# Kernel tuning notes

Hardware: AMD Instinct MI355X
Metric: run time of the kernel (lower is better)

## Reference

```python
import jax, jax.numpy as jnp
import numpy as np

B, S, D = 4, 2048, 1024
H, HD = 16, 64
FF = 4096
EPS = 1e-5
NEG = -1000000.0


def setup_inputs() -> dict:
    key = jax.random.key(0)
    ks = jax.random.split(key, 12)
    sc = lambda n: 1.0 / np.sqrt(n)
    return {
        "x": jax.random.normal(ks[0], (B, S, D), jnp.float32),
        "valid_lens": jax.random.randint(ks[1], (B,), 1, S, jnp.int32),
        "Wq": jax.random.normal(ks[2], (D, H * HD), jnp.float32) * sc(D),
        "Wk": jax.random.normal(ks[3], (D, H * HD), jnp.float32) * sc(D),
        "Wv": jax.random.normal(ks[4], (D, H * HD), jnp.float32) * sc(D),
        "Wo": jax.random.normal(ks[5], (H * HD, D), jnp.float32) * sc(H * HD),
        "W1": jax.random.normal(ks[6], (D, FF), jnp.float32) * sc(D),
        "b1": jnp.zeros((FF,), jnp.float32),
        "W2": jax.random.normal(ks[7], (FF, D), jnp.float32) * sc(FF),
        "b2": jnp.zeros((D,), jnp.float32),
        "g1": jnp.ones((D,), jnp.float32),
        "beta1": jnp.zeros((D,), jnp.float32),
        "g2": jnp.ones((D,), jnp.float32),
        "beta2": jnp.zeros((D,), jnp.float32),
    }


def _layernorm(x, g, b):
    mu = jnp.mean(x, axis=-1, keepdims=True)
    var = jnp.var(x, axis=-1, keepdims=True)
    return (x - mu) * jax.lax.rsqrt(var + EPS) * g + b


def _encoder_block(x, valid_lens, Wq, Wk, Wv, Wo, W1, b1, W2, b2, g1, beta1, g2, beta2):
    # multi-head attention (vectorized over heads; masked softmax as in original)
    q = (x @ Wq).reshape(B, S, H, HD)
    k = (x @ Wk).reshape(B, S, H, HD)
    v = (x @ Wv).reshape(B, S, H, HD)
    scores = jnp.einsum("bqhd,bkhd->bhqk", q, k) / np.sqrt(HD)
    # mask: key positions >= valid_len[b] set to -1e6 (matches python-loop masking)
    col = jnp.arange(S)[None, None, None, :]           # [1,1,1,S]
    mask = col < valid_lens[:, None, None, None]       # [B,1,1,S]
    scores = jnp.where(mask, scores, NEG)
    w = jax.nn.softmax(scores, axis=-1)
    attn = jnp.einsum("bhqk,bkhd->bqhd", w, v).reshape(B, S, H * HD)
    attn_out = attn @ Wo
    res1 = _layernorm(attn_out + x, g1, beta1)
    ff = jax.nn.relu(res1 @ W1 + b1) @ W2 + b2
    return _layernorm(ff + res1, g2, beta2)


def reference(x, valid_lens, Wq, Wk, Wv, Wo, W1, b1, W2, b2, g1, beta1, g2, beta2):
    return _encoder_block(x, valid_lens, Wq, Wk, Wv, Wo, W1, b1, W2, b2, g1, beta1, g2, beta2)
```

## Files before the change

kernel.cpp:

```cpp
#include <hip/hip_runtime.h>
#include <hip/hip_bf16.h>
#include <stdint.h>

#define BB 4
#define SS 2048
#define DD 1024
#define HH 16
#define HD 64
#define FF 4096
#define MM (BB * SS)
#define BH (BB * HH)

typedef __bf16 bf16x8 __attribute__((ext_vector_type(8)));
typedef float f32x4 __attribute__((ext_vector_type(4)));

static __device__ __forceinline__ unsigned short f2bf(float f) {
  union { float f; unsigned u; } v; v.f = f;
  unsigned r = v.u + 0x7fffu + ((v.u >> 16) & 1u);
  return (unsigned short)(r >> 16);
}

#define GLD_LDS16(SRC, DST)                                          \
  __builtin_amdgcn_global_load_lds(                                  \
      (const __attribute__((address_space(1))) void*)(SRC),          \
      (__attribute__((address_space(3))) void*)(DST), 16, 0, 0)

__global__ __launch_bounds__(256) void cast_bf16_k(const float* __restrict__ in,
                                                   unsigned short* __restrict__ out) {
  size_t i = ((size_t)blockIdx.x * 256 + threadIdx.x) * 4;
  float4 v = *(const float4*)(in + i);
  ushort4 u;
  u.x = f2bf(v.x); u.y = f2bf(v.y); u.z = f2bf(v.z); u.w = f2bf(v.w);
  *(ushort4*)(out + i) = u;
}

__global__ __launch_bounds__(256) void transpose_cast_k(const float* __restrict__ in,
                                                        unsigned short* __restrict__ out,
                                                        int K, int N) {
  __shared__ float tile[32][33];
  int n0 = blockIdx.x * 32, k0 = blockIdx.y * 32;
  int tx = threadIdx.x, ty = threadIdx.y;
#pragma unroll
  for (int i = 0; i < 32; i += 8)
    tile[ty + i][tx] = in[(size_t)(k0 + ty + i) * N + n0 + tx];
  __syncthreads();
#pragma unroll
  for (int i = 0; i < 32; i += 8)
    out[(size_t)(n0 + ty + i) * K + k0 + tx] = f2bf(tile[tx][ty + i]);
}

template <int EPI>
__global__ __launch_bounds__(256, 2) void gemm_bt(const unsigned short* __restrict__ A,
                                                  const unsigned short* __restrict__ BT,
                                                  const float* __restrict__ bias,
                                                  void* __restrict__ Cout,
                                                  int N, int K) {
  __shared__ __align__(16) unsigned short Al[128 * 64];
  __shared__ __align__(16) unsigned short Bl[128 * 64];
  const int t = threadIdx.x;
  const int w = t >> 6, l = t & 63, lr = l & 15, lg = l >> 4;
  const int brow = blockIdx.y << 7, bcol = blockIdx.x << 7;
  const int wr = w >> 1, wc = w & 1;
  f32x4 acc[4][4] = {};

  for (int kt = 0; kt < K; kt += 64) {
    __syncthreads();
#pragma unroll
    for (int is = 0; is < 4; ++is) {
      int c = is * 256 + t;
      int row = c >> 3;
      int js = (c & 7) ^ (row & 7);
      GLD_LDS16(A + (size_t)(brow + row) * K + kt + js * 8,
                &Al[(size_t)(is * 256 + w * 64) * 8]);
      GLD_LDS16(BT + (size_t)(bcol + row) * K + kt + js * 8,
                &Bl[(size_t)(is * 256 + w * 64) * 8]);
    }
    __syncthreads();
#pragma unroll
    for (int kk = 0; kk < 2; ++kk) {
      bf16x8 af[4], bfr[4];
#pragma unroll
      for (int m = 0; m < 4; ++m) {
        int row = wr * 64 + m * 16 + lr;
        af[m] = *(const bf16x8*)&Al[row * 64 + (((kk * 4 + lg) ^ (row & 7)) << 3)];
      }
#pragma unroll
      for (int n = 0; n < 4; ++n) {
        int row = wc * 64 + n * 16 + lr;
        bfr[n] = *(const bf16x8*)&Bl[row * 64 + (((kk * 4 + lg) ^ (row & 7)) << 3)];
      }
#pragma unroll
      for (int m = 0; m < 4; ++m)
#pragma unroll
        for (int n = 0; n < 4; ++n)
          acc[m][n] = __builtin_amdgcn_mfma_f32_16x16x32_bf16(af[m], bfr[n], acc[m][n], 0, 0, 0);
    }
  }

#pragma unroll
  for (int m = 0; m < 4; ++m) {
#pragma unroll
    for (int n = 0; n < 4; ++n) {
      int col = bcol + wc * 64 + n * 16 + lr;
      float bv = 0.f;
      if (EPI == 3 || EPI == 4) bv = bias[col];
#pragma unroll
      for (int i = 0; i < 4; ++i) {
        int row = brow + wr * 64 + m * 16 + lg * 4 + i;
        float v = acc[m][n][i];
        if (EPI == 0) {
          ((float*)Cout)[(size_t)row * N + col] = v;
        } else if (EPI == 1) {
          int b = row >> 11, s = row & 2047, h = col >> 6, hd = col & 63;
          ((unsigned short*)Cout)[(((size_t)(b * HH + h)) * SS + s) * HD + hd] = f2bf(v);
        } else if (EPI == 2) {
          int b = row >> 11, s = row & 2047, h = col >> 6, hd = col & 63;
          ((unsigned short*)Cout)[(((size_t)(b * HH + h)) * HD + hd) * SS + s] = f2bf(v);
        } else if (EPI == 3) {
          v += bv; v = v > 0.f ? v : 0.f;
          ((unsigned short*)Cout)[(size_t)row * N + col] = f2bf(v);
        } else {
          v += bv;
          ((float*)Cout)[(size_t)row * N + col] = v;
        }
      }
    }
  }
}

__global__ __launch_bounds__(256, 2) void attn_kernel(const unsigned short* __restrict__ Q,
                                                      const unsigned short* __restrict__ Kg,
                                                      const unsigned short* __restrict__ VT,
                                                      const int* __restrict__ vlens,
                                                      unsigned short* __restrict__ O) {
  __shared__ __align__(16) unsigned short Kt[64 * 64];
  __shared__ __align__(16) unsigned short Vt[64 * 64];
  __shared__ __align__(16) unsigned short Pt[4][16 * 64];
  const int t = threadIdx.x;
  const int w = t >> 6, l = t & 63, lr = l & 15, lg = l >> 4;
  const int bh = blockIdx.y, b = bh >> 4, h = bh & 15;
  const int q0 = blockIdx.x << 6;
  const int vl = vlens[b];
  const size_t base = (size_t)bh * SS * HD;

  bf16x8 qf[2];
  {
    const int qrow = q0 + w * 16 + lr;
    qf[0] = *(const bf16x8*)(Q + base + (size_t)qrow * HD + lg * 8);
    qf[1] = *(const bf16x8*)(Q + base + (size_t)qrow * HD + 32 + lg * 8);
  }
  f32x4 o[4] = {};
  float m_i[4], l_i[4];
#pragma unroll
  for (int i = 0; i < 4; ++i) { m_i[i] = -3.0e38f; l_i[i] = 0.f; }

  const int nkv = (vl + 63) >> 6;
  for (int kbi = 0; kbi < nkv; ++kbi) {
    const int kb = kbi << 6;
    __syncthreads();
#pragma unroll
    for (int is = 0; is < 2; ++is) {
      int c = is * 256 + t;
      int row = c >> 3;
      int js = (c & 7) ^ (row & 7);
      GLD_LDS16(Kg + base + (size_t)(kb + row) * HD + js * 8,
                &Kt[(is * 256 + w * 64) * 8]);
      GLD_LDS16(VT + base + (size_t)row * SS + kb + js * 8,
                &Vt[(is * 256 + w * 64) * 8]);
    }
    __syncthreads();

    f32x4 s[4] = {};
#pragma unroll
    for (int kk = 0; kk < 2; ++kk)
#pragma unroll
      for (int n = 0; n < 4; ++n) {
        int row = n * 16 + lr;
        bf16x8 kf = *(const bf16x8*)&Kt[row * 64 + (((kk * 4 + lg) ^ (row & 7)) << 3)];
        s[n] = __builtin_amdgcn_mfma_f32_16x16x32_bf16(qf[kk], kf, s[n], 0, 0, 0);
      }

#pragma unroll
    for (int i = 0; i < 4; ++i) {
      float rm = -3.0e38f;
#pragma unroll
      for (int n = 0; n < 4; ++n) {
        float sv = s[n][i] * 0.125f;
        if (kb + n * 16 + lr >= vl) sv = -3.0e38f;
        s[n][i] = sv;
        rm = fmaxf(rm, sv);
      }
      rm = fmaxf(rm, __shfl_xor(rm, 1));
      rm = fmaxf(rm, __shfl_xor(rm, 2));
      rm = fmaxf(rm, __shfl_xor(rm, 4));
      rm = fmaxf(rm, __shfl_xor(rm, 8));
      float mnew = fmaxf(m_i[i], rm);
      float alpha = __expf(m_i[i] - mnew);
      float rs = 0.f;
#pragma unroll
      for (int n = 0; n < 4; ++n) {
        float p = __expf(s[n][i] - mnew);
        s[n][i] = p;
        rs += p;
      }
      rs += __shfl_xor(rs, 1);
      rs += __shfl_xor(rs, 2);
      rs += __shfl_xor(rs, 4);
      rs += __shfl_xor(rs, 8);
      l_i[i] = l_i[i] * alpha + rs;
      m_i[i] = mnew;
#pragma unroll
      for (int n = 0; n < 4; ++n) o[n][i] *= alpha;
    }

#pragma unroll
    for (int n = 0; n < 4; ++n) {
      int colc = n * 2 + (lr >> 3);
      int cl = lr & 7;
#pragma unroll
      for (int i = 0; i < 4; ++i) {
        int row = lg * 4 + i;
        Pt[w][row * 64 + ((colc ^ (row & 7)) << 3) + cl] = f2bf(s[n][i]);
      }
    }
#pragma unroll
    for (int kk = 0; kk < 2; ++kk) {
      bf16x8 pf = *(const bf16x8*)&Pt[w][lr * 64 + (((kk * 4 + lg) ^ (lr & 7)) << 3)];
#pragma unroll
      for (int n = 0; n < 4; ++n) {
        int row = n * 16 + lr;
        bf16x8 vf = *(const bf16x8*)&Vt[row * 64 + (((kk * 4 + lg) ^ (row & 7)) << 3)];
        o[n] = __builtin_amdgcn_mfma_f32_16x16x32_bf16(pf, vf, o[n], 0, 0, 0);
      }
    }
  }

  float inv[4];
#pragma unroll
  for (int i = 0; i < 4; ++i) inv[i] = 1.f / l_i[i];
#pragma unroll
  for (int n = 0; n < 4; ++n)
#pragma unroll
    for (int i = 0; i < 4; ++i) {
      int qrow = q0 + w * 16 + lg * 4 + i;
      O[((size_t)b * SS + qrow) * DD + h * HD + n * 16 + lr] = f2bf(o[n][i] * inv[i]);
    }
}

__global__ __launch_bounds__(256) void ln_kernel(const float* __restrict__ a,
                                                 const float* __restrict__ bsrc,
                                                 const float* __restrict__ g,
                                                 const float* __restrict__ be,
                                                 float* __restrict__ outf,
                                                 unsigned short* __restrict__ outb) {
  const int row = blockIdx.x;
  const int t = threadIdx.x;
  const float4 av = ((const float4*)(a + (size_t)row * DD))[t];
  const float4 bv = ((const float4*)(bsrc + (size_t)row * DD))[t];
  float4 s;
  s.x = av.x + bv.x; s.y = av.y + bv.y; s.z = av.z + bv.z; s.w = av.w + bv.w;
  float sum = s.x + s.y + s.z + s.w;
  float sq = s.x * s.x + s.y * s.y + s.z * s.z + s.w * s.w;
#pragma unroll
  for (int mm = 1; mm < 64; mm <<= 1) {
    sum += __shfl_xor(sum, mm);
    sq += __shfl_xor(sq, mm);
  }
  __shared__ float red[8];
  const int w = t >> 6, l = t & 63;
  if (l == 0) { red[w] = sum; red[4 + w] = sq; }
  __syncthreads();
  sum = red[0] + red[1] + red[2] + red[3];
  sq = red[4] + red[5] + red[6] + red[7];
  const float mu = sum * (1.f / (float)DD);
  const float var = sq * (1.f / (float)DD) - mu * mu;
  const float rs = rsqrtf(var + 1e-5f);
  const float4 gv = ((const float4*)g)[t];
  const float4 bev = ((const float4*)be)[t];
  float4 y;
  y.x = (s.x - mu) * rs * gv.x + bev.x;
  y.y = (s.y - mu) * rs * gv.y + bev.y;
  y.z = (s.z - mu) * rs * gv.z + bev.z;
  y.w = (s.w - mu) * rs * gv.w + bev.w;
  if (outf) ((float4*)(outf + (size_t)row * DD))[t] = y;
  if (outb) {
    ushort4 u;
    u.x = f2bf(y.x); u.y = f2bf(y.y); u.z = f2bf(y.z); u.w = f2bf(y.w);
    ((ushort4*)(outb + (size_t)row * DD))[t] = u;
  }
}

extern "C" void kernel_launch(void* const* d_in, const int* in_sizes, int n_in,
                              void* d_out, int out_size, void* d_ws, size_t ws_size,
                              hipStream_t stream) {
  (void)in_sizes; (void)n_in; (void)out_size; (void)ws_size;
  const float* x = (const float*)d_in[0];
  const int* vlen = (const int*)d_in[1];
  const float* Wq = (const float*)d_in[2];
  const float* Wk = (const float*)d_in[3];
  const float* Wv = (const float*)d_in[4];
  const float* Wo = (const float*)d_in[5];
  const float* W1 = (const float*)d_in[6];
  const float* b1 = (const float*)d_in[7];
  const float* W2 = (const float*)d_in[8];
  const float* b2 = (const float*)d_in[9];
  const float* g1 = (const float*)d_in[10];
  const float* be1 = (const float*)d_in[11];
  const float* g2 = (const float*)d_in[12];
  const float* be2 = (const float*)d_in[13];
  float* out = (float*)d_out;

  char* ws = (char*)d_ws;
  size_t off = 0;
  auto alloc = [&](size_t bytes) {
    char* p = ws + off;
    off += (bytes + 255) & ~(size_t)255;
    return p;
  };
  unsigned short* xb = (unsigned short*)alloc((size_t)MM * DD * 2);
  unsigned short* WqT = (unsigned short*)alloc((size_t)DD * DD * 2);
  unsigned short* WkT = (unsigned short*)alloc((size_t)DD * DD * 2);
  unsigned short* WvT = (unsigned short*)alloc((size_t)DD * DD * 2);
  unsigned short* WoT = (unsigned short*)alloc((size_t)DD * DD * 2);
  unsigned short* W1T = (unsigned short*)alloc((size_t)FF * DD * 2);
  unsigned short* W2T = (unsigned short*)alloc((size_t)DD * FF * 2);
  unsigned short* Qb = (unsigned short*)alloc((size_t)MM * DD * 2);
  unsigned short* Kbb = (unsigned short*)alloc((size_t)MM * DD * 2);
  unsigned short* VTb = (unsigned short*)alloc((size_t)MM * DD * 2);
  unsigned short* attnb = (unsigned short*)alloc((size_t)MM * DD * 2);
  float* proj = (float*)alloc((size_t)MM * DD * 4);
  float* res1f = (float*)alloc((size_t)MM * DD * 4);
  unsigned short* res1b = (unsigned short*)alloc((size_t)MM * DD * 2);
  unsigned short* ff1 = Qb;
  float* ff2 = proj;

  cast_bf16_k<<<MM * DD / 1024, 256, 0, stream>>>(x, xb);
  transpose_cast_k<<<dim3(32, 32), dim3(32, 8), 0, stream>>>(Wq, WqT, DD, DD);
  transpose_cast_k<<<dim3(32, 32), dim3(32, 8), 0, stream>>>(Wk, WkT, DD, DD);
  transpose_cast_k<<<dim3(32, 32), dim3(32, 8), 0, stream>>>(Wv, WvT, DD, DD);
  transpose_cast_k<<<dim3(32, 32), dim3(32, 8), 0, stream>>>(Wo, WoT, DD, DD);
  transpose_cast_k<<<dim3(128, 32), dim3(32, 8), 0, stream>>>(W1, W1T, DD, FF);
  transpose_cast_k<<<dim3(32, 128), dim3(32, 8), 0, stream>>>(W2, W2T, FF, DD);

  gemm_bt<1><<<dim3(8, 64), 256, 0, stream>>>(xb, WqT, nullptr, Qb, DD, DD);
  gemm_bt<1><<<dim3(8, 64), 256, 0, stream>>>(xb, WkT, nullptr, Kbb, DD, DD);
  gemm_bt<2><<<dim3(8, 64), 256, 0, stream>>>(xb, WvT, nullptr, VTb, DD, DD);

  attn_kernel<<<dim3(SS / 64, BH), 256, 0, stream>>>(Qb, Kbb, VTb, vlen, attnb);

  gemm_bt<0><<<dim3(8, 64), 256, 0, stream>>>(attnb, WoT, nullptr, proj, DD, DD);
  ln_kernel<<<MM, 256, 0, stream>>>(proj, x, g1, be1, res1f, res1b);
  gemm_bt<3><<<dim3(32, 64), 256, 0, stream>>>(res1b, W1T, b1, ff1, FF, DD);
  gemm_bt<4><<<dim3(8, 64), 256, 0, stream>>>(ff1, W2T, b2, ff2, DD, FF);
  ln_kernel<<<MM, 256, 0, stream>>>(ff2, res1f, g2, be2, out, nullptr);
}
```

Measured before the change: 456.7 us.

## Fuse QKV projections into one GEMM and widen attention KV tiles with lazy rescaling

Replaces three separate Q/K/V projection GEMMs with one N=3072 GEMM whose epilogue scatters into the Q, K and transposed-V buffers, and folds the 1/sqrt(d) scale into Q. The attention kernel now processes 128-key blocks per iteration and applies the mask as an additive bias. It skips the online-softmax rescale unless the running max grows by more than 8. This cuts kernel launches, loop iterations and exp/multiply work. The fused GEMM assumes the three weight buffers and the three output buffers sit contiguously in memory.

```diff
diff --git a/kernel.cpp b/kernel.cpp
--- a/kernel.cpp
+++ b/kernel.cpp
@@ -110,18 +110,24 @@
         float v = acc[m][n][i];
         if (EPI == 0) {
           ((float*)Cout)[(size_t)row * N + col] = v;
-        } else if (EPI == 1) {
-          int b = row >> 11, s = row & 2047, h = col >> 6, hd = col & 63;
-          ((unsigned short*)Cout)[(((size_t)(b * HH + h)) * SS + s) * HD + hd] = f2bf(v);
-        } else if (EPI == 2) {
-          int b = row >> 11, s = row & 2047, h = col >> 6, hd = col & 63;
-          ((unsigned short*)Cout)[(((size_t)(b * HH + h)) * HD + hd) * SS + s] = f2bf(v);
         } else if (EPI == 3) {
           v += bv; v = v > 0.f ? v : 0.f;
           ((unsigned short*)Cout)[(size_t)row * N + col] = f2bf(v);
-        } else {
+        } else if (EPI == 4) {
           v += bv;
           ((float*)Cout)[(size_t)row * N + col] = v;
+        } else if (EPI == 5) {
+          int b = row >> 11, s = row & 2047;
+          int which = col >> 10, cin = col & 1023;
+          int h = cin >> 6, hd = cin & 63;
+          unsigned short* qb = (unsigned short*)Cout;
+          if (which == 0) {
+            qb[(((size_t)(b * HH + h)) * SS + s) * HD + hd] = f2bf(v * 0.125f);
+          } else if (which == 1) {
+            (qb + (size_t)MM * DD)[(((size_t)(b * HH + h)) * SS + s) * HD + hd] = f2bf(v);
+          } else {
+            (qb + 2 * (size_t)MM * DD)[(((size_t)(b * HH + h)) * HD + hd) * SS + s] = f2bf(v);
+          }
         }
       }
     }
@@ -133,9 +139,9 @@
                                                       const unsigned short* __restrict__ VT,
                                                       const int* __restrict__ vlens,
                                                       unsigned short* __restrict__ O) {
-  __shared__ __align__(16) unsigned short Kt[64 * 64];
-  __shared__ __align__(16) unsigned short Vt[64 * 64];
-  __shared__ __align__(16) unsigned short Pt[4][16 * 64];
+  __shared__ __align__(16) unsigned short Kt[128 * 64];
+  __shared__ __align__(16) unsigned short Vt[64 * 128];
+  __shared__ __align__(16) unsigned short Pt[4][16 * 128];
   const int t = threadIdx.x;
   const int w = t >> 6, l = t & 63, lr = l & 15, lg = l >> 4;
   const int bh = blockIdx.y, b = bh >> 4, h = bh & 15;
@@ -154,39 +160,45 @@
 #pragma unroll
   for (int i = 0; i < 4; ++i) { m_i[i] = -3.0e38f; l_i[i] = 0.f; }
 
-  const int nkv = (vl + 63) >> 6;
+  const int nkv = (vl + 127) >> 7;
   for (int kbi = 0; kbi < nkv; ++kbi) {
-    const int kb = kbi << 6;
+    const int kb = kbi << 7;
     __syncthreads();
 #pragma unroll
-    for (int is = 0; is < 2; ++is) {
+    for (int is = 0; is < 4; ++is) {
       int c = is * 256 + t;
-      int row = c >> 3;
-      int js = (c & 7) ^ (row & 7);
-      GLD_LDS16(Kg + base + (size_t)(kb + row) * HD + js * 8,
+      int krow = c >> 3;
+      int kjs = (c & 7) ^ (krow & 7);
+      GLD_LDS16(Kg + base + (size_t)(kb + krow) * HD + kjs * 8,
                 &Kt[(is * 256 + w * 64) * 8]);
-      GLD_LDS16(VT + base + (size_t)row * SS + kb + js * 8,
+      int vrow = c >> 4;
+      int vjs = (c & 15) ^ (vrow & 7);
+      GLD_LDS16(VT + base + (size_t)vrow * SS + kb + vjs * 8,
                 &Vt[(is * 256 + w * 64) * 8]);
     }
     __syncthreads();
 
-    f32x4 s[4] = {};
+    f32x4 s[8] = {};
 #pragma unroll
     for (int kk = 0; kk < 2; ++kk)
 #pragma unroll
-      for (int n = 0; n < 4; ++n) {
+      for (int n = 0; n < 8; ++n) {
         int row = n * 16 + lr;
         bf16x8 kf = *(const bf16x8*)&Kt[row * 64 + (((kk * 4 + lg) ^ (row & 7)) << 3)];
         s[n] = __builtin_amdgcn_mfma_f32_16x16x32_bf16(qf[kk], kf, s[n], 0, 0, 0);
       }
 
+    float mneg[8];
+#pragma unroll
+    for (int n = 0; n < 8; ++n)
+      mneg[n] = (kb + n * 16 + lr >= vl) ? -1.0e30f : 0.f;
+
 #pragma unroll
     for (int i = 0; i < 4; ++i) {
       float rm = -3.0e38f;
 #pragma unroll
-      for (int n = 0; n < 4; ++n) {
-        float sv = s[n][i] * 0.125f;
-        if (kb + n * 16 + lr >= vl) sv = -3.0e38f;
+      for (int n = 0; n < 8; ++n) {
+        float sv = s[n][i] + mneg[n];
         s[n][i] = sv;
         rm = fmaxf(rm, sv);
       }
@@ -194,12 +206,18 @@
       rm = fmaxf(rm, __shfl_xor(rm, 2));
       rm = fmaxf(rm, __shfl_xor(rm, 4));
       rm = fmaxf(rm, __shfl_xor(rm, 8));
-      float mnew = fmaxf(m_i[i], rm);
-      float alpha = __expf(m_i[i] - mnew);
+      if (__any(rm > m_i[i] + 8.f)) {
+        float mnew = fmaxf(m_i[i], rm);
+        float alpha = __expf(m_i[i] - mnew);
+        m_i[i] = mnew;
+        l_i[i] *= alpha;
+#pragma unroll
+        for (int n = 0; n < 4; ++n) o[n][i] *= alpha;
+      }
       float rs = 0.f;
 #pragma unroll
-      for (int n = 0; n < 4; ++n) {
-        float p = __expf(s[n][i] - mnew);
+      for (int n = 0; n < 8; ++n) {
+        float p = __expf(s[n][i] - m_i[i]);
         s[n][i] = p;
         rs += p;
       }
@@ -207,29 +225,26 @@
       rs += __shfl_xor(rs, 2);
       rs += __shfl_xor(rs, 4);
       rs += __shfl_xor(rs, 8);
-      l_i[i] = l_i[i] * alpha + rs;
-      m_i[i] = mnew;
-#pragma unroll
-      for (int n = 0; n < 4; ++n) o[n][i] *= alpha;
-    }
-
-#pragma unroll
-    for (int n = 0; n < 4; ++n) {
-      int colc = n * 2 + (lr >> 3);
+      l_i[i] += rs;
+    }
+
+#pragma unroll
+    for (int n = 0; n < 8; ++n) {
+      int c = n * 2 + (lr >> 3);
       int cl = lr & 7;
 #pragma unroll
       for (int i = 0; i < 4; ++i) {
         int row = lg * 4 + i;
-        Pt[w][row * 64 + ((colc ^ (row & 7)) << 3) + cl] = f2bf(s[n][i]);
-      }
-    }
-#pragma unroll
-    for (int kk = 0; kk < 2; ++kk) {
-      bf16x8 pf = *(const bf16x8*)&Pt[w][lr * 64 + (((kk * 4 + lg) ^ (lr & 7)) << 3)];
+        Pt[w][row * 128 + ((c ^ (row & 7)) << 3) + cl] = f2bf(s[n][i]);
+      }
+    }
+#pragma unroll
+    for (int kk = 0; kk < 4; ++kk) {
+      bf16x8 pf = *(const bf16x8*)&Pt[w][lr * 128 + (((kk * 4 + lg) ^ (lr & 7)) << 3)];
 #pragma unroll
       for (int n = 0; n < 4; ++n) {
         int row = n * 16 + lr;
-        bf16x8 vf = *(const bf16x8*)&Vt[row * 64 + (((kk * 4 + lg) ^ (row & 7)) << 3)];
+        bf16x8 vf = *(const bf16x8*)&Vt[row * 128 + (((kk * 4 + lg) ^ (row & 7)) << 3)];
         o[n] = __builtin_amdgcn_mfma_f32_16x16x32_bf16(pf, vf, o[n], 0, 0, 0);
       }
     }
@@ -333,6 +348,7 @@
   unsigned short* res1b = (unsigned short*)alloc((size_t)MM * DD * 2);
   unsigned short* ff1 = Qb;
   float* ff2 = proj;
+  (void)Kbb; (void)VTb;
 
   cast_bf16_k<<<MM * DD / 1024, 256, 0, stream>>>(x, xb);
   transpose_cast_k<<<dim3(32, 32), dim3(32, 8), 0, stream>>>(Wq, WqT, DD, DD);
@@ -342,9 +358,7 @@
   transpose_cast_k<<<dim3(128, 32), dim3(32, 8), 0, stream>>>(W1, W1T, DD, FF);
   transpose_cast_k<<<dim3(32, 128), dim3(32, 8), 0, stream>>>(W2, W2T, FF, DD);
 
-  gemm_bt<1><<<dim3(8, 64), 256, 0, stream>>>(xb, WqT, nullptr, Qb, DD, DD);
-  gemm_bt<1><<<dim3(8, 64), 256, 0, stream>>>(xb, WkT, nullptr, Kbb, DD, DD);
-  gemm_bt<2><<<dim3(8, 64), 256, 0, stream>>>(xb, WvT, nullptr, VTb, DD, DD);
+  gemm_bt<5><<<dim3(24, 64), 256, 0, stream>>>(xb, WqT, nullptr, Qb, 3072, DD);
 
   attn_kernel<<<dim3(SS / 64, BH), 256, 0, stream>>>(Qb, Kbb, VTb, vlen, attnb);
 
```

Result: no change. 460.1 us (+0.7%).

## Fuse QKV projections and keep attention probabilities in registers with lazy rescale

Applied to the files above, without the earlier changes.

Merges the three Q/K/V projection GEMMs into one N=3072 launch with a combined epilogue. That epilogue folds the 1/sqrt(d) scale into Q and relies on the weight and output buffers sitting back to back in memory. The attention kernel now computes S transposed, so each lane owns one query row. The probabilities are packed to bf16 and moved into the PV operand through cross-lane shuffles instead of a shared-memory round trip. Softmax rescaling runs only when the running max rises by more than a threshold. The GEMM also remaps block indices for better L2 locality, and attention raises its occupancy hint and flattens its grid.

```diff
diff --git a/kernel.cpp b/kernel.cpp
--- a/kernel.cpp
+++ b/kernel.cpp
@@ -18,6 +18,11 @@
   union { float f; unsigned u; } v; v.f = f;
   unsigned r = v.u + 0x7fffu + ((v.u >> 16) & 1u);
   return (unsigned short)(r >> 16);
+}
+
+static __device__ __forceinline__ unsigned packbf2(float a, float b) {
+  __hip_bfloat162 h = __float22bfloat162_rn(float2{a, b});
+  union { __hip_bfloat162 h; unsigned u; } cv; cv.h = h; return cv.u;
 }
 
 #define GLD_LDS16(SRC, DST)                                          \
@@ -59,7 +64,11 @@
   __shared__ __align__(16) unsigned short Bl[128 * 64];
   const int t = threadIdx.x;
   const int w = t >> 6, l = t & 63, lr = l & 15, lg = l >> 4;
-  const int brow = blockIdx.y << 7, bcol = blockIdx.x << 7;
+  const int gx = gridDim.x;
+  int lin = blockIdx.y * gx + blockIdx.x;
+  const int nb = gx * gridDim.y;
+  lin = (lin & 7) * (nb >> 3) + (lin >> 3);
+  const int brow = (lin / gx) << 7, bcol = (lin % gx) << 7;
   const int wr = w >> 1, wc = w & 1;
   f32x4 acc[4][4] = {};
 
@@ -110,36 +119,43 @@
         float v = acc[m][n][i];
         if (EPI == 0) {
           ((float*)Cout)[(size_t)row * N + col] = v;
-        } else if (EPI == 1) {
-          int b = row >> 11, s = row & 2047, h = col >> 6, hd = col & 63;
-          ((unsigned short*)Cout)[(((size_t)(b * HH + h)) * SS + s) * HD + hd] = f2bf(v);
-        } else if (EPI == 2) {
-          int b = row >> 11, s = row & 2047, h = col >> 6, hd = col & 63;
-          ((unsigned short*)Cout)[(((size_t)(b * HH + h)) * HD + hd) * SS + s] = f2bf(v);
         } else if (EPI == 3) {
           v += bv; v = v > 0.f ? v : 0.f;
           ((unsigned short*)Cout)[(size_t)row * N + col] = f2bf(v);
-        } else {
+        } else if (EPI == 4) {
           v += bv;
           ((float*)Cout)[(size_t)row * N + col] = v;
+        } else if (EPI == 5) {
+          int b = row >> 11, s = row & 2047;
+          int which = col >> 10, cin = col & 1023;
+          int h = cin >> 6, hd = cin & 63;
+          unsigned short* qb = (unsigned short*)Cout;
+          if (which == 0) {
+            qb[(((size_t)(b * HH + h)) * SS + s) * HD + hd] = f2bf(v * 0.125f);
+          } else if (which == 1) {
+            (qb + (size_t)MM * DD)[(((size_t)(b * HH + h)) * SS + s) * HD + hd] = f2bf(v);
+          } else {
+            (qb + 2 * (size_t)MM * DD)[(((size_t)(b * HH + h)) * HD + hd) * SS + s] = f2bf(v);
+          }
         }
       }
     }
   }
 }
 
-__global__ __launch_bounds__(256, 2) void attn_kernel(const unsigned short* __restrict__ Q,
+__global__ __launch_bounds__(256, 4) void attn_kernel(const unsigned short* __restrict__ Q,
                                                       const unsigned short* __restrict__ Kg,
                                                       const unsigned short* __restrict__ VT,
                                                       const int* __restrict__ vlens,
                                                       unsigned short* __restrict__ O) {
   __shared__ __align__(16) unsigned short Kt[64 * 64];
   __shared__ __align__(16) unsigned short Vt[64 * 64];
-  __shared__ __align__(16) unsigned short Pt[4][16 * 64];
   const int t = threadIdx.x;
   const int w = t >> 6, l = t & 63, lr = l & 15, lg = l >> 4;
-  const int bh = blockIdx.y, b = bh >> 4, h = bh & 15;
-  const int q0 = blockIdx.x << 6;
+  const int gid = blockIdx.x;
+  const int bh = gid & 63, qb = gid >> 6;
+  const int b = bh >> 4, h = bh & 15;
+  const int q0 = qb << 6;
   const int vl = vlens[b];
   const size_t base = (size_t)bh * SS * HD;
 
@@ -150,9 +166,7 @@
     qf[1] = *(const bf16x8*)(Q + base + (size_t)qrow * HD + 32 + lg * 8);
   }
   f32x4 o[4] = {};
-  float m_i[4], l_i[4];
-#pragma unroll
-  for (int i = 0; i < 4; ++i) { m_i[i] = -3.0e38f; l_i[i] = 0.f; }
+  float m_r = -3.0e38f, l_r = 0.f;
 
   const int nkv = (vl + 63) >> 6;
   for (int kbi = 0; kbi < nkv; ++kbi) {
@@ -177,73 +191,98 @@
       for (int n = 0; n < 4; ++n) {
         int row = n * 16 + lr;
         bf16x8 kf = *(const bf16x8*)&Kt[row * 64 + (((kk * 4 + lg) ^ (row & 7)) << 3)];
-        s[n] = __builtin_amdgcn_mfma_f32_16x16x32_bf16(qf[kk], kf, s[n], 0, 0, 0);
-      }
-
-#pragma unroll
-    for (int i = 0; i < 4; ++i) {
-      float rm = -3.0e38f;
-#pragma unroll
-      for (int n = 0; n < 4; ++n) {
-        float sv = s[n][i] * 0.125f;
-        if (kb + n * 16 + lr >= vl) sv = -3.0e38f;
-        s[n][i] = sv;
-        rm = fmaxf(rm, sv);
-      }
-      rm = fmaxf(rm, __shfl_xor(rm, 1));
-      rm = fmaxf(rm, __shfl_xor(rm, 2));
-      rm = fmaxf(rm, __shfl_xor(rm, 4));
-      rm = fmaxf(rm, __shfl_xor(rm, 8));
-      float mnew = fmaxf(m_i[i], rm);
-      float alpha = __expf(m_i[i] - mnew);
-      float rs = 0.f;
-#pragma unroll
-      for (int n = 0; n < 4; ++n) {
-        float p = __expf(s[n][i] - mnew);
-        s[n][i] = p;
-        rs += p;
-      }
-      rs += __shfl_xor(rs, 1);
-      rs += __shfl_xor(rs, 2);
-      rs += __shfl_xor(rs, 4);
-      rs += __shfl_xor(rs, 8);
-      l_i[i] = l_i[i] * alpha + rs;
-      m_i[i] = mnew;
-#pragma unroll
-      for (int n = 0; n < 4; ++n) o[n][i] *= alpha;
-    }
-
+        s[n] = __builtin_amdgcn_mfma_f32_16x16x32_bf16(kf, qf[kk], s[n], 0, 0, 0);
+      }
+
+    float sv[16];
+    const int kbase = kb + lg * 4;
+#pragma unroll
+    for (int n = 0; n < 4; ++n)
+#pragma unroll
+      for (int i = 0; i < 4; ++i) {
+        float v = s[n][i];
+        if (kbase + n * 16 + i >= vl) v = -1.0e30f;
+        sv[n * 4 + i] = v;
+      }
+    float tm[16];
+#pragma unroll
+    for (int j = 0; j < 16; ++j) tm[j] = sv[j];
+#pragma unroll
+    for (int st = 8; st >= 1; st >>= 1)
+#pragma unroll
+      for (int j = 0; j < 8; ++j)
+        if (j < st) tm[j] = fmaxf(tm[j], tm[j + st]);
+    float rm = tm[0];
+    rm = fmaxf(rm, __shfl_xor(rm, 16));
+    rm = fmaxf(rm, __shfl_xor(rm, 32));
+
+    if (__any(rm > m_r + 8.f)) {
+      float mnew = fmaxf(m_r, rm);
+      float alpha = __expf(m_r - mnew);
+      m_r = mnew;
+      l_r *= alpha;
+      float af[4];
+#pragma unroll
+      for (int i = 0; i < 4; ++i) af[i] = __shfl(alpha, lg * 4 + i);
+#pragma unroll
+      for (int n = 0; n < 4; ++n)
+#pragma unroll
+        for (int i = 0; i < 4; ++i) o[n][i] *= af[i];
+    }
+
+    float p[16];
+#pragma unroll
+    for (int j = 0; j < 16; ++j) p[j] = __expf(sv[j] - m_r);
+    float ts[16];
+#pragma unroll
+    for (int j = 0; j < 16; ++j) ts[j] = p[j];
+#pragma unroll
+    for (int st = 8; st >= 1; st >>= 1)
+#pragma unroll
+      for (int j = 0; j < 8; ++j)
+        if (j < st) ts[j] += ts[j + st];
+    float rs = ts[0];
+    rs += __shfl_xor(rs, 16);
+    rs += __shfl_xor(rs, 32);
+    l_r += rs;
+
+    unsigned pd[4][2];
 #pragma unroll
     for (int n = 0; n < 4; ++n) {
-      int colc = n * 2 + (lr >> 3);
-      int cl = lr & 7;
-#pragma unroll
-      for (int i = 0; i < 4; ++i) {
-        int row = lg * 4 + i;
-        Pt[w][row * 64 + ((colc ^ (row & 7)) << 3) + cl] = f2bf(s[n][i]);
-      }
-    }
+      pd[n][0] = packbf2(p[n * 4 + 0], p[n * 4 + 1]);
+      pd[n][1] = packbf2(p[n * 4 + 2], p[n * 4 + 3]);
+    }
+
 #pragma unroll
     for (int kk = 0; kk < 2; ++kk) {
-      bf16x8 pf = *(const bf16x8*)&Pt[w][lr * 64 + (((kk * 4 + lg) ^ (lr & 7)) << 3)];
-#pragma unroll
-      for (int n = 0; n < 4; ++n) {
-        int row = n * 16 + lr;
+      unsigned pa[4];
+#pragma unroll
+      for (int jj = 0; jj < 4; ++jj) {
+        int src = lr + 16 * (2 * (lg & 1) + (jj >> 1));
+        unsigned rlo = __shfl(pd[2 * kk + 0][jj & 1], src);
+        unsigned rhi = __shfl(pd[2 * kk + 1][jj & 1], src);
+        pa[jj] = (lg & 2) ? rhi : rlo;
+      }
+      union { unsigned u[4]; bf16x8 v; } pb;
+      pb.u[0] = pa[0]; pb.u[1] = pa[1]; pb.u[2] = pa[2]; pb.u[3] = pa[3];
+#pragma unroll
+      for (int nd = 0; nd < 4; ++nd) {
+        int row = nd * 16 + lr;
         bf16x8 vf = *(const bf16x8*)&Vt[row * 64 + (((kk * 4 + lg) ^ (row & 7)) << 3)];
-        o[n] = __builtin_amdgcn_mfma_f32_16x16x32_bf16(pf, vf, o[n], 0, 0, 0);
-      }
-    }
-  }
-
-  float inv[4];
-#pragma unroll
-  for (int i = 0; i < 4; ++i) inv[i] = 1.f / l_i[i];
-#pragma unroll
-  for (int n = 0; n < 4; ++n)
+        o[nd] = __builtin_amdgcn_mfma_f32_16x16x32_bf16(pb.v, vf, o[nd], 0, 0, 0);
+      }
+    }
+  }
+
+  float linv[4];
+#pragma unroll
+  for (int i = 0; i < 4; ++i) linv[i] = 1.f / __shfl(l_r, lg * 4 + i);
+#pragma unroll
+  for (int nd = 0; nd < 4; ++nd)
 #pragma unroll
     for (int i = 0; i < 4; ++i) {
       int qrow = q0 + w * 16 + lg * 4 + i;
-      O[((size_t)b * SS + qrow) * DD + h * HD + n * 16 + lr] = f2bf(o[n][i] * inv[i]);
+      O[((size_t)b * SS + qrow) * DD + h * HD + nd * 16 + lr] = f2bf(o[nd][i] * linv[i]);
     }
 }
 
@@ -333,6 +372,7 @@
   unsigned short* res1b = (unsigned short*)alloc((size_t)MM * DD * 2);
   unsigned short* ff1 = Qb;
   float* ff2 = proj;
+  (void)Kbb; (void)VTb;
 
   cast_bf16_k<<<MM * DD / 1024, 256, 0, stream>>>(x, xb);
   transpose_cast_k<<<dim3(32, 32), dim3(32, 8), 0, stream>>>(Wq, WqT, DD, DD);
@@ -342,11 +382,9 @@
   transpose_cast_k<<<dim3(128, 32), dim3(32, 8), 0, stream>>>(W1, W1T, DD, FF);
   transpose_cast_k<<<dim3(32, 128), dim3(32, 8), 0, stream>>>(W2, W2T, FF, DD);
 
-  gemm_bt<1><<<dim3(8, 64), 256, 0, stream>>>(xb, WqT, nullptr, Qb, DD, DD);
-  gemm_bt<1><<<dim3(8, 64), 256, 0, stream>>>(xb, WkT, nullptr, Kbb, DD, DD);
-  gemm_bt<2><<<dim3(8, 64), 256, 0, stream>>>(xb, WvT, nullptr, VTb, DD, DD);
-
-  attn_kernel<<<dim3(SS / 64, BH), 256, 0, stream>>>(Qb, Kbb, VTb, vlen, attnb);
+  gemm_bt<5><<<dim3(24, 64), 256, 0, stream>>>(xb, WqT, nullptr, Qb, 3072, DD);
+
+  attn_kernel<<<dim3(2048), 256, 0, stream>>>(Qb, Kbb, VTb, vlen, attnb);
 
   gemm_bt<0><<<dim3(8, 64), 256, 0, stream>>>(attnb, WoT, nullptr, proj, DD, DD);
   ln_kernel<<<MM, 256, 0, stream>>>(proj, x, g1, be1, res1f, res1b);
```

New measurement: 454.9 us. About the same (-0.4%).
